# Kernel optimization log

Hardware: AMD Instinct MI355X
Metric: run time of the kernel (lower is better)

Reference implementation:

```python
import jax, jax.numpy as jnp
import numpy as np

N = 16384            # mesh vertices at full resolution (level 3)
DEG = 8              # avg nonzeros per Laplacian row
F_IN = 3
F_HID = 128
LOCAL_LAYERS = 15
LEVEL_N = [N >> (3 - l) for l in range(4)]  # [2048, 4096, 8192, 16384]


def setup_inputs():
    key = jax.random.key(0)
    ks = iter(jax.random.split(key, 48))
    d = {}
    d['inputs'] = jax.random.normal(next(ks), (1, N, F_IN), dtype=jnp.float32)
    d['mask0'] = jnp.ones((1, N, 1), jnp.float32)
    d['mask1'] = jnp.ones((1, N, 1), jnp.float32)
    for l, n in enumerate(LEVEL_N):
        e = DEG * n
        d[f'lap{l}_rows'] = jnp.sort(jax.random.randint(next(ks), (e,), 0, n, dtype=jnp.int32))
        d[f'lap{l}_cols'] = jax.random.randint(next(ks), (e,), 0, n, dtype=jnp.int32)
        d[f'lap{l}_vals'] = 0.25 * jax.random.normal(next(ks), (e,), dtype=jnp.float32)
    e = DEG * N
    d['L_rows'] = jnp.sort(jax.random.randint(next(ks), (e,), 0, N, dtype=jnp.int32))
    d['L_cols'] = jax.random.randint(next(ks), (e,), 0, N, dtype=jnp.int32)
    d['L_vals'] = 0.25 * jax.random.normal(next(ks), (e,), dtype=jnp.float32)
    s_in = 0.577   # ~1/sqrt(F_IN)
    s_h = 0.0625   # 1/sqrt(2*F_HID)
    d['g_conv1_W'] = s_in * jax.random.normal(next(ks), (F_IN, F_HID), dtype=jnp.float32)
    d['g_conv1_b'] = jnp.zeros((F_HID,), jnp.float32)
    d['g_down_W'] = s_h * jax.random.normal(next(ks), (3, 2, 2 * F_HID, F_HID), dtype=jnp.float32)
    d['g_down_b'] = jnp.zeros((3, 2, F_HID), jnp.float32)
    d['g_lap0_W'] = s_h * jax.random.normal(next(ks), (2, 2 * F_HID, F_HID), dtype=jnp.float32)
    d['g_lap0_b'] = jnp.zeros((2, F_HID), jnp.float32)
    d['g_up_W'] = s_h * jax.random.normal(next(ks), (3, 2, 2 * F_HID, F_HID), dtype=jnp.float32)
    d['g_up_b'] = jnp.zeros((3, 2, F_HID), jnp.float32)
    d['g_conv2_W'] = s_h * jax.random.normal(next(ks), (F_HID, 2), dtype=jnp.float32)
    d['g_conv2_b'] = jnp.zeros((2,), jnp.float32)
    d['l_conv1_W'] = s_in * jax.random.normal(next(ks), (F_IN, F_HID), dtype=jnp.float32)
    d['l_conv1_b'] = jnp.zeros((F_HID,), jnp.float32)
    d['l_rn_W'] = s_h * jax.random.normal(next(ks), (LOCAL_LAYERS, 2, 2 * F_HID, F_HID), dtype=jnp.float32)
    d['l_rn_b'] = jnp.zeros((LOCAL_LAYERS, 2, F_HID), jnp.float32)
    d['l_conv2_W'] = s_h * jax.random.normal(next(ks), (F_HID, 1), dtype=jnp.float32)
    d['l_conv2_b'] = jnp.zeros((1,), jnp.float32)
    return d


def _spmm(rows, cols, vals, x):
    # y = L @ x for an n x n COO Laplacian; x: [1, n, f] (batch=1, sparse mm path)
    y = jax.ops.segment_sum(vals[:, None] * x[0, cols, :], rows, num_segments=x.shape[1])
    return y[None]


def _lap_block(lap, x, Ws, bs):
    # _LapResNet2 (num_outputs == num_inputs == 128): elu -> cat([x, Lx]) -> 1x1 conv, residual
    inp = x
    for j in range(Ws.shape[0]):
        x = jax.nn.elu(x)
        x = jnp.concatenate([x, _spmm(lap[0], lap[1], lap[2], x)], axis=-1) @ Ws[j] + bs[j]
    return x + inp


def _avg_block(mask, x, Ws, bs):
    # _AvgResNet2: elu -> cat([x, masked global average]) -> 1x1 conv, residual
    inp = x
    denom = jnp.sum(mask, axis=1, keepdims=True)
    for j in range(Ws.shape[0]):
        x = jax.nn.elu(x)
        avg = jnp.sum(x * mask, axis=1, keepdims=True) / denom
        x = jnp.concatenate([x, jnp.broadcast_to(avg, x.shape)], axis=-1) @ Ws[j] + bs[j]
    return x + inp


def _maxpool2(x):
    # MaxPool1d(2, stride=2) along the node dim
    b, n, f = x.shape
    return x.reshape(b, n // 2, 2, f).max(axis=2)


def _forward(inputs, mask0, mask1, lap0_vals, lap1_vals, lap2_vals, lap3_vals, L_vals,
             g_conv1_W, g_conv1_b, g_down_W, g_down_b, g_lap0_W, g_lap0_b,
             g_up_W, g_up_b, g_conv2_W, g_conv2_b,
             l_conv1_W, l_conv1_b, l_rn_W, l_rn_b, l_conv2_W, l_conv2_b,
             lap0_rows, lap0_cols, lap1_rows, lap1_cols, lap2_rows, lap2_cols,
             lap3_rows, lap3_cols, L_rows, L_cols):
    laps = [(lap0_rows, lap0_cols, lap0_vals), (lap1_rows, lap1_cols, lap1_vals),
            (lap2_rows, lap2_cols, lap2_vals), (lap3_rows, lap3_cols, lap3_vals)]
    # ----- global net: EfficientCascade (naive max-pool cascade, 4 levels) -----
    # (mask0 is only max-pooled in torch; _LapResNet2 ignores it, so it does not affect math)
    x = inputs @ g_conv1_W + g_conv1_b
    down = []
    for k, i in enumerate((3, 2, 1)):
        down.append(x)
        x = _lap_block(laps[i], x, g_down_W[k], g_down_b[k])
        x = _maxpool2(x)
    x = _lap_block(laps[0], x, g_lap0_W, g_lap0_b)
    for i in (1, 2, 3):
        x = jnp.repeat(x, 2, axis=1)      # F.interpolate(scale_factor=2), nearest
        x = x + down[-i]                  # channels equal -> plain residual add
        x = _lap_block(laps[i], x, g_up_W[i - 1], g_up_b[i - 1])
    swg = jax.nn.elu(x) @ g_conv2_W + g_conv2_b + inputs[:, :, :2]  # + repeating_expand(inputs, 2)
    # ----- local net: LapDeepModel, 15 alternating Lap / global-avg resblocks -----
    L = (L_rows, L_cols, L_vals)
    y = inputs @ l_conv1_W + l_conv1_b
    for i in range(LOCAL_LAYERS):
        if i % 2 == 0:
            y = _lap_block(L, y, l_rn_W[i], l_rn_b[i])
        else:
            y = _avg_block(mask1, y, l_rn_W[i], l_rn_b[i])
    score_local = jax.nn.elu(y) @ l_conv2_W + l_conv2_b + inputs[:, :, :1]
    # ----- combine -----
    score_global = swg[:, :, :1]
    weight_global = jax.nn.sigmoid(swg[:, :, :-1])  # out_features=1 -> same first channel
    score_final = weight_global * score_global + (1.0 - weight_global) * score_local
    return jnp.concatenate([score_global, score_local, score_final], axis=1)


def reference(inputs, mask0, mask1, lap0_rows, lap0_cols, lap0_vals,
              lap1_rows, lap1_cols, lap1_vals, lap2_rows, lap2_cols, lap2_vals,
              lap3_rows, lap3_cols, lap3_vals, L_rows, L_cols, L_vals,
              g_conv1_W, g_conv1_b, g_down_W, g_down_b, g_lap0_W, g_lap0_b,
              g_up_W, g_up_b, g_conv2_W, g_conv2_b,
              l_conv1_W, l_conv1_b, l_rn_W, l_rn_b, l_conv2_W, l_conv2_b):
    return _forward(inputs, mask0, mask1, lap0_vals, lap1_vals, lap2_vals, lap3_vals, L_vals,
                    g_conv1_W, g_conv1_b, g_down_W, g_down_b, g_lap0_W, g_lap0_b,
                    g_up_W, g_up_b, g_conv2_W, g_conv2_b,
                    l_conv1_W, l_conv1_b, l_rn_W, l_rn_b, l_conv2_W, l_conv2_b,
                    lap0_rows, lap0_cols, lap1_rows, lap1_cols, lap2_rows, lap2_cols,
                    lap3_rows, lap3_cols, L_rows, L_cols)
```

## Files before the change

kernel.cpp:

```cpp
#include <hip/hip_runtime.h>

#define F 128
#define SPAD 136
#define NR 32

typedef __attribute__((ext_vector_type(8))) short short8;
typedef __attribute__((ext_vector_type(16))) float f32x16;
typedef unsigned long long ull;

__device__ __forceinline__ float elu_f(float x) {
    return x > 0.f ? x : __expf(x) - 1.f;
}
__device__ __forceinline__ ushort f2bf(float x) {
    unsigned u = __float_as_uint(x);
    u = (u + 0x7FFFu + ((u >> 16) & 1u)) >> 16;
    return (ushort)u;
}
__device__ __forceinline__ float bf2f(ushort u) {
    return __uint_as_float((unsigned)u << 16);
}
__device__ __forceinline__ void bfma8(float* a, float v, short8 u) {
#pragma unroll
    for (int i = 0; i < 8; ++i) a[i] += v * bf2f((ushort)u[i]);
}

struct SetupArgs {
    const float* ws0; const float* ws1; const float* ws2; const float* ws3;
    ushort* wd0; ushort* wd1; ushort* wd2; ushort* wd3;
    const int* rows0; const int* rows1; const int* rows2; const int* rows3; const int* rows4;
    int* rp0; int* rp1; int* rp2; int* rp3; int* rp4;
    const float* mask; float* den; float* acc;
    const float* in; const float* Wg; const float* bg; const float* Wl; const float* bl;
    float* og; ushort* eg; float* ol; ushort* el;
};

__global__ __launch_bounds__(256) void setup_conv1(SetupArgs s) {
    __shared__ ushort tile[16384];
    int b = blockIdx.x, t = threadIdx.x;
    if (b >= 274) {
        int id = (b - 274) * 256 + t;
        int r = id >> 7, c = id & 127;
        float x0 = s.in[r * 3 + 0], x1 = s.in[r * 3 + 1], x2 = s.in[r * 3 + 2];
        float g = x0 * s.Wg[c] + x1 * s.Wg[F + c] + x2 * s.Wg[2 * F + c] + s.bg[c];
        float lo = x0 * s.Wl[c] + x1 * s.Wl[F + c] + x2 * s.Wl[2 * F + c] + s.bl[c];
        s.og[id] = g;  s.eg[id] = f2bf(elu_f(g));
        s.ol[id] = lo; s.el[id] = f2bf(elu_f(lo));
    } else if (b < 88) {
        const float* src; ushort* dst; int lb;
        if (b < 12)      { src = s.ws0; dst = s.wd0; lb = b; }
        else if (b < 16) { src = s.ws1; dst = s.wd1; lb = b - 12; }
        else if (b < 28) { src = s.ws2; dst = s.wd2; lb = b - 16; }
        else             { src = s.ws3; dst = s.wd3; lb = b - 28; }
        src += (size_t)lb * 16384; dst += (size_t)lb * 16384;
        for (int idx = t; idx < 16384; idx += 256) {
            int k = idx >> 7, nn = idx & 127;
            int k0 = k >> 4, rk = k & 15, j = rk & 7, lh = rk >> 3;
            int n0 = nn >> 5, ll = nn & 31;
            tile[((k0 * 4 + n0) * 64 + lh * 32 + ll) * 8 + j] = f2bf(src[idx]);
        }
        __syncthreads();
        ull* td = (ull*)dst; const ull* ts = (const ull*)tile;
        for (int i = t; i < 4096; i += 256) td[i] = ts[i];
    } else if (b < 273) {
        int tid = (b - 88) * 256 + t;
        const int ns[5] = {2048, 4096, 8192, 16384, 16384};
        const int es[5] = {16384, 32768, 65536, 131072, 131072};
        const int* rowsA[5] = {s.rows0, s.rows1, s.rows2, s.rows3, s.rows4};
        int* rpA[5] = {s.rp0, s.rp1, s.rp2, s.rp3, s.rp4};
        int base = 0;
        for (int lv = 0; lv < 5; ++lv) {
            int cnt = ns[lv] + 1;
            if (tid < base + cnt) {
                int r = tid - base;
                const int* rows = rowsA[lv]; int e = es[lv];
                int lo = 0, hi = e;
                while (lo < hi) { int mid = (lo + hi) >> 1; if (rows[mid] < r) lo = mid + 1; else hi = mid; }
                rpA[lv][r] = lo;
                return;
            }
            base += cnt;
        }
    } else {
        __shared__ float red[256];
        float ssum = 0.f;
        for (int i = t; i < 16384; i += 256) ssum += s.mask[i];
        red[t] = ssum; __syncthreads();
        for (int st = 128; st > 0; st >>= 1) { if (t < st) red[t] += red[t + st]; __syncthreads(); }
        if (t == 0) s.den[0] = red[0];
        for (int i = t; i < 14336; i += 256) s.acc[i] = 0.f;
    }
}

struct LArgs {
    const ushort* EA; const float* RES; float* OUT; ushort* EAOUT;
    const int* rowptr; const int* cols; const float* vals;
    const ushort* Wp; const float* bias;
    const float* accin; const float* den;
    const float* mask; float* accout;
    float* EO; ushort* EE; const float* SKIP;
    int epi;
    int fin;
    const float* Finp; const ushort* FEB0;
    const float* FgW2; const float* Fgb2; const float* FlW2; const float* Flb2;
    float* Fout;
};

__device__ __forceinline__ void layer_body(const LArgs& a, int blk, ushort* SS, float* FS) {
    const int t = threadIdx.x;
    const int rbase = blk * NR;
    const int w = t >> 6, l = t & 63, m = l & 31, kh = l >> 5;
    const int col = w * 32 + m;
    const bool lap = (a.rowptr != nullptr);
    const bool avg = (a.accin != nullptr);

    short8 afrag[8];
    {
        const ushort* ear = a.EA + (size_t)(rbase + m) * F + kh * 8;
#pragma unroll
        for (int ki = 0; ki < 8; ++ki) afrag[ki] = *(const short8*)(ear + ki * 16);
    }

    if (lap) {
        const int grp = t >> 3, l8 = t & 7;
        const short8* EA8 = (const short8*)a.EA;
        const int chunk = l8 * 2;
        int row = rbase + grp;
        int e0 = a.rowptr[row], e1 = a.rowptr[row + 1];
        float acc0[16], acc1[16];
#pragma unroll
        for (int i = 0; i < 16; ++i) { acc0[i] = 0.f; acc1[i] = 0.f; }
        int e = e0;
        for (; e + 4 <= e1; e += 4) {
            int c0 = a.cols[e + 0], c1 = a.cols[e + 1], c2 = a.cols[e + 2], c3 = a.cols[e + 3];
            float v0 = a.vals[e + 0], v1 = a.vals[e + 1], v2 = a.vals[e + 2], v3 = a.vals[e + 3];
            short8 u0a = EA8[(size_t)c0 * 16 + chunk], u0b = EA8[(size_t)c0 * 16 + chunk + 1];
            short8 u1a = EA8[(size_t)c1 * 16 + chunk], u1b = EA8[(size_t)c1 * 16 + chunk + 1];
            short8 u2a = EA8[(size_t)c2 * 16 + chunk], u2b = EA8[(size_t)c2 * 16 + chunk + 1];
            short8 u3a = EA8[(size_t)c3 * 16 + chunk], u3b = EA8[(size_t)c3 * 16 + chunk + 1];
            bfma8(acc0, v0, u0a); bfma8(acc0 + 8, v0, u0b);
            bfma8(acc1, v1, u1a); bfma8(acc1 + 8, v1, u1b);
            bfma8(acc0, v2, u2a); bfma8(acc0 + 8, v2, u2b);
            bfma8(acc1, v3, u3a); bfma8(acc1 + 8, v3, u3b);
        }
        for (; e < e1; ++e) {
            int cc = a.cols[e];
            float v = a.vals[e];
            short8 ua = EA8[(size_t)cc * 16 + chunk], ub = EA8[(size_t)cc * 16 + chunk + 1];
            bfma8(acc0, v, ua); bfma8(acc0 + 8, v, ub);
        }
        short8 s0, s1;
#pragma unroll
        for (int i = 0; i < 8; ++i) {
            s0[i] = (short)f2bf(acc0[i] + acc1[i]);
            s1[i] = (short)f2bf(acc0[8 + i] + acc1[8 + i]);
        }
        *(short8*)(&SS[grp * SPAD + l8 * 16]) = s0;
        *(short8*)(&SS[grp * SPAD + l8 * 16 + 8]) = s1;
        __syncthreads();
    } else if (avg) {
        if (t < 128) {
            float s = 0.f;
#pragma unroll
            for (int r = 0; r < 8; ++r) s += a.accin[r * 128 + t];
            SS[t] = f2bf(s / a.den[0]);
        }
        __syncthreads();
    }

    f32x16 acc;
#pragma unroll
    for (int i = 0; i < 16; ++i) acc[i] = 0.f;
#pragma unroll
    for (int ki = 0; ki < 8; ++ki) {
        short8 b = *(const short8*)(a.Wp + (size_t)(((ki * 4 + w) * 64 + l) * 8));
        acc = __builtin_amdgcn_mfma_f32_32x32x16_bf16(afrag[ki], b, acc, 0, 0, 0);
    }
    if (lap || avg) {
        const ushort* esr = lap ? &SS[m * SPAD + kh * 8] : &SS[kh * 8];
#pragma unroll
        for (int ki = 0; ki < 8; ++ki) {
            short8 aa = *(const short8*)(esr + ki * 16);
            short8 b = *(const short8*)(a.Wp + 16384 + (size_t)(((ki * 4 + w) * 64 + l) * 8));
            acc = __builtin_amdgcn_mfma_f32_32x32x16_bf16(aa, b, acc, 0, 0, 0);
        }
    }

    const float bv = a.bias[col];
    float outv[16];
#pragma unroll
    for (int reg = 0; reg < 16; ++reg) {
        int r = (reg & 3) + 8 * (reg >> 2) + 4 * kh;
        size_t rg = (size_t)(rbase + r);
        float v = acc[reg] + bv;
        if (a.RES) v += a.RES[rg * F + col];
        outv[reg] = v;
        if (a.OUT) a.OUT[rg * F + col] = v;
        if (a.EAOUT) a.EAOUT[rg * F + col] = f2bf(elu_f(v));
    }
    if (a.accout) {
        float p = 0.f;
#pragma unroll
        for (int reg = 0; reg < 16; ++reg) {
            int r = (reg & 3) + 8 * (reg >> 2) + 4 * kh;
            p += elu_f(outv[reg]) * a.mask[rbase + r];
        }
        p += __shfl_xor(p, 32, 64);
        if (l < 32) atomicAdd(a.accout + (blk & 7) * 128 + col, p);
    }
    if (a.epi == 1) {
        int rb2 = rbase >> 1;
#pragma unroll
        for (int q = 0; q < 4; ++q)
#pragma unroll
            for (int e2 = 0; e2 < 2; ++e2) {
                float pv = fmaxf(outv[q * 4 + e2 * 2], outv[q * 4 + e2 * 2 + 1]);
                size_t idx = (size_t)(rb2 + q * 4 + kh * 2 + e2) * F + col;
                a.EO[idx] = pv;
                a.EE[idx] = f2bf(elu_f(pv));
            }
    } else if (a.epi == 2) {
#pragma unroll
        for (int reg = 0; reg < 16; ++reg) {
            int r = (reg & 3) + 8 * (reg >> 2) + 4 * kh;
            size_t R0 = (size_t)(2 * (rbase + r)) * F + col;
            float v0 = outv[reg] + a.SKIP[R0];
            float v1 = outv[reg] + a.SKIP[R0 + F];
            a.EO[R0] = v0;     a.EO[R0 + F] = v1;
            a.EE[R0] = f2bf(elu_f(v0)); a.EE[R0 + F] = f2bf(elu_f(v1));
        }
    }
    if (a.fin) {
        __syncthreads();
        if (t < 64) FS[t] = 0.f;
        __syncthreads();
        const float lw = a.FlW2[col];
#pragma unroll
        for (int reg = 0; reg < 16; ++reg) {
            int r = (reg & 3) + 8 * (reg >> 2) + 4 * kh;
            atomicAdd(&FS[r], elu_f(outv[reg]) * lw);
        }
        for (int idx = t; idx < 32 * 128; idx += 256) {
            int r = idx >> 7, cc = idx & 127;
            atomicAdd(&FS[32 + r], bf2f(a.FEB0[(size_t)(rbase + r) * F + cc]) * a.FgW2[2 * cc]);
        }
        __syncthreads();
        if (t < 32) {
            int rg = rbase + t;
            float base = a.Finp[rg * 3 + 0];
            float sg = FS[32 + t] + a.Fgb2[0] + base;
            float sl = FS[t] + a.Flb2[0] + base;
            float wg = 1.f / (1.f + __expf(-sg));
            a.Fout[rg] = sg;
            a.Fout[16384 + rg] = sl;
            a.Fout[32768 + rg] = wg * sg + (1.f - wg) * sl;
        }
    }
}

__global__ __launch_bounds__(256)
void dual_layer(LArgs A, LArgs B, int nA) {
    __shared__ ushort SS[NR * SPAD];
    __shared__ float FS[64];
    bool isA = (int)blockIdx.x < nA;
    const LArgs& a = isA ? A : B;
    int blk = isA ? blockIdx.x : blockIdx.x - nA;
    layer_body(a, blk, SS, FS);
}

extern "C" void kernel_launch(void* const* d_in, const int* in_sizes, int n_in,
                              void* d_out, int out_size, void* d_ws, size_t ws_size,
                              hipStream_t stream) {
    (void)in_sizes; (void)n_in; (void)out_size; (void)ws_size;
    const float* inputs = (const float*)d_in[0];
    const float* mask1  = (const float*)d_in[2];
    const int*   lrows[5] = {(const int*)d_in[3], (const int*)d_in[6], (const int*)d_in[9],
                             (const int*)d_in[12], (const int*)d_in[15]};
    const int*   lcols[5] = {(const int*)d_in[4], (const int*)d_in[7], (const int*)d_in[10],
                             (const int*)d_in[13], (const int*)d_in[16]};
    const float* lvals[5] = {(const float*)d_in[5], (const float*)d_in[8], (const float*)d_in[11],
                             (const float*)d_in[14], (const float*)d_in[17]};
    const float* gW1 = (const float*)d_in[18];
    const float* gb1 = (const float*)d_in[19];
    const float* gdW = (const float*)d_in[20];
    const float* gdb = (const float*)d_in[21];
    const float* glW = (const float*)d_in[22];
    const float* glb = (const float*)d_in[23];
    const float* guW = (const float*)d_in[24];
    const float* gub = (const float*)d_in[25];
    const float* gW2 = (const float*)d_in[26];
    const float* gb2 = (const float*)d_in[27];
    const float* lW1 = (const float*)d_in[28];
    const float* lb1 = (const float*)d_in[29];
    const float* lrW = (const float*)d_in[30];
    const float* lrb = (const float*)d_in[31];
    const float* lW2 = (const float*)d_in[32];
    const float* lb2 = (const float*)d_in[33];
    float* out = (float*)d_out;

    const int N = 16384;
    const int nlev[5] = {2048, 4096, 8192, 16384, 16384};

    char* ws = (char*)d_ws;
    size_t off = 0;
    auto alloc = [&](size_t bytes) -> char* {
        char* p = ws + off;
        off = (off + bytes + 255) & ~(size_t)255;
        return p;
    };
    float* BUF0 = (float*)alloc((size_t)N * F * 4);
    float* GU   = (float*)alloc((size_t)N * F * 4);
    float* G2   = (float*)alloc((size_t)N * F * 4);
    float* D8   = (float*)alloc((size_t)8192 * F * 4);
    float* D4   = (float*)alloc((size_t)4096 * F * 4);
    float* D2   = (float*)alloc((size_t)2048 * F * 4);
    float* LB   = (float*)alloc((size_t)N * F * 4);
    ushort* EB0 = (ushort*)alloc((size_t)N * F * 2);
    ushort* EG1 = (ushort*)alloc((size_t)N * F * 2);
    ushort* EG2 = (ushort*)alloc((size_t)N * F * 2);
    ushort* ED8 = (ushort*)alloc((size_t)8192 * F * 2);
    ushort* ED4 = (ushort*)alloc((size_t)4096 * F * 2);
    ushort* ED2 = (ushort*)alloc((size_t)2048 * F * 2);
    ushort* LE1 = (ushort*)alloc((size_t)N * F * 2);
    ushort* LE2 = (ushort*)alloc((size_t)N * F * 2);
    int* rp[5];
    for (int i = 0; i < 5; ++i) rp[i] = (int*)alloc((size_t)(nlev[i] + 1) * 4);
    float* ACC = (float*)alloc((size_t)14 * 8 * 128 * 4);
    float* DEN = (float*)alloc(4);
    ushort* Pd = (ushort*)alloc((size_t)12 * 16384 * 2);
    ushort* Pl = (ushort*)alloc((size_t)4  * 16384 * 2);
    ushort* Pu = (ushort*)alloc((size_t)12 * 16384 * 2);
    ushort* Pr = (ushort*)alloc((size_t)60 * 16384 * 2);

    SetupArgs sa;
    sa.ws0 = gdW; sa.ws1 = glW; sa.ws2 = guW; sa.ws3 = lrW;
    sa.wd0 = Pd;  sa.wd1 = Pl;  sa.wd2 = Pu;  sa.wd3 = Pr;
    sa.rows0 = lrows[0]; sa.rows1 = lrows[1]; sa.rows2 = lrows[2];
    sa.rows3 = lrows[3]; sa.rows4 = lrows[4];
    sa.rp0 = rp[0]; sa.rp1 = rp[1]; sa.rp2 = rp[2]; sa.rp3 = rp[3]; sa.rp4 = rp[4];
    sa.mask = mask1; sa.den = DEN; sa.acc = ACC;
    sa.in = inputs; sa.Wg = gW1; sa.bg = gb1; sa.Wl = lW1; sa.bl = lb1;
    sa.og = BUF0; sa.eg = EB0; sa.ol = LB; sa.el = LE1;
    setup_conv1<<<274 + 8192, 256, 0, stream>>>(sa);

    const size_t PSZ = 2 * 16384;

    auto mkL = [&](const ushort* ea, const float* res, float* o, ushort* eao,
                   int lv, const ushort* wp, const float* bias, float* accout,
                   int epi, float* eo, ushort* ee, const float* skip,
                   const float* accin, int fin) {
        LArgs x;
        x.EA = ea; x.RES = res; x.OUT = o; x.EAOUT = eao;
        x.rowptr = (lv >= 0) ? rp[lv] : nullptr;
        x.cols = (lv >= 0) ? lcols[lv] : nullptr;
        x.vals = (lv >= 0) ? lvals[lv] : nullptr;
        x.Wp = wp; x.bias = bias;
        x.accin = accin; x.den = DEN;
        x.mask = mask1; x.accout = accout;
        x.EO = eo; x.EE = ee; x.SKIP = skip; x.epi = epi;
        x.fin = fin;
        x.Finp = inputs; x.FEB0 = EB0;
        x.FgW2 = gW2; x.Fgb2 = gb2; x.FlW2 = lW2; x.Flb2 = lb2; x.Fout = out;
        return x;
    };

    LArgs gs[14]; int gn[14];
    gs[0]  = mkL(EB0, 0, 0, EG1, 3, Pd + 0 * PSZ, gdb + 0,   0, 0, 0, 0, 0, 0, 0);  gn[0]  = 16384;
    gs[1]  = mkL(EG1, BUF0, 0, 0, 3, Pd + 1 * PSZ, gdb + 128, 0, 1, D8, ED8, 0, 0, 0); gn[1] = 16384;
    gs[2]  = mkL(ED8, 0, 0, EG1, 2, Pd + 2 * PSZ, gdb + 256, 0, 0, 0, 0, 0, 0, 0);  gn[2]  = 8192;
    gs[3]  = mkL(EG1, D8, 0, 0, 2, Pd + 3 * PSZ, gdb + 384, 0, 1, D4, ED4, 0, 0, 0); gn[3]  = 8192;
    gs[4]  = mkL(ED4, 0, 0, EG1, 1, Pd + 4 * PSZ, gdb + 512, 0, 0, 0, 0, 0, 0, 0);  gn[4]  = 4096;
    gs[5]  = mkL(EG1, D4, 0, 0, 1, Pd + 5 * PSZ, gdb + 640, 0, 1, D2, ED2, 0, 0, 0); gn[5]  = 4096;
    gs[6]  = mkL(ED2, 0, 0, EG1, 0, Pl + 0 * PSZ, glb + 0,   0, 0, 0, 0, 0, 0, 0);  gn[6]  = 2048;
    gs[7]  = mkL(EG1, D2, 0, 0, 0, Pl + 1 * PSZ, glb + 128, 0, 2, GU, EG2, D4, 0, 0); gn[7] = 2048;
    gs[8]  = mkL(EG2, 0, 0, EG1, 1, Pu + 0 * PSZ, gub + 0,   0, 0, 0, 0, 0, 0, 0);  gn[8]  = 4096;
    gs[9]  = mkL(EG1, GU, 0, 0, 1, Pu + 1 * PSZ, gub + 128, 0, 2, G2, EG2, D8, 0, 0); gn[9] = 4096;
    gs[10] = mkL(EG2, 0, 0, EG1, 2, Pu + 2 * PSZ, gub + 256, 0, 0, 0, 0, 0, 0, 0);  gn[10] = 8192;
    gs[11] = mkL(EG1, G2, 0, 0, 2, Pu + 3 * PSZ, gub + 384, 0, 2, GU, EG2, BUF0, 0, 0); gn[11] = 8192;
    gs[12] = mkL(EG2, 0, 0, EG1, 3, Pu + 4 * PSZ, gub + 512, 0, 0, 0, 0, 0, 0, 0);  gn[12] = 16384;
    gs[13] = mkL(EG1, GU, 0, EB0, 3, Pu + 5 * PSZ, gub + 640, 0, 0, 0, 0, 0, 0, 0); gn[13] = 16384;

    int gi = 0;
    auto launchLap = [&](const LArgs& loc) {
        if (gi < 14) {
            int na = gn[gi] / NR;
            dual_layer<<<na + 512, 256, 0, stream>>>(gs[gi], loc, na);
            ++gi;
        } else {
            dual_layer<<<512, 256, 0, stream>>>(loc, loc, 512);
        }
    };

    for (int i = 0; i < 15; ++i) {
        const ushort* P1 = Pr + (size_t)(2 * i) * PSZ;
        const ushort* P2 = Pr + (size_t)(2 * i + 1) * PSZ;
        const float* b1 = lrb + (size_t)i * 256;
        const float* b2 = b1 + 128;
        if ((i & 1) == 0) {
            LArgs s1 = mkL(LE1, 0, 0, LE2, 4, P1, b1, 0, 0, 0, 0, 0, 0, 0);
            float* accout = (i <= 12) ? (ACC + (size_t)i * 1024) : nullptr;
            int fin = (i == 14);
            LArgs s2 = mkL(LE2, LB, fin ? nullptr : LB, fin ? nullptr : LE1, 4,
                           P2, b2, accout, 0, 0, 0, 0, 0, fin);
            launchLap(s1);
            launchLap(s2);
        } else {
            LArgs s1 = mkL(LE1, 0, 0, LE2, -1, P1, b1, ACC + (size_t)i * 1024,
                           0, 0, 0, 0, ACC + (size_t)(i - 1) * 1024, 0);
            LArgs s2 = mkL(LE2, LB, LB, LE1, -1, P2, b2, 0,
                           0, 0, 0, 0, ACC + (size_t)i * 1024, 0);
            launchLap(s1);
            launchLap(s2);
        }
    }
}
```

Baseline: 680.1 us.

## Stage Laplacian neighbor rows into LDS via global_load_lds before SpMM

Replaces the per-thread direct gather of bf16 neighbor rows in the sparse Laplacian product with a block-cooperative staging scheme. Each wave issues global_load_lds for chunks of 112 edges into a shared buffer, then threads accumulate from LDS. The aim is to turn scattered vector loads into asynchronous direct-to-LDS transfers. In exchange it adds about 30KB of LDS per block, extra barriers per chunk, and serial shuffle-driven issue, which may cut occupancy. A buffer named GU is renamed to avoid clashing with a new typedef.

```diff
diff --git a/kernel.cpp b/kernel.cpp
--- a/kernel.cpp
+++ b/kernel.cpp
@@ -3,10 +3,15 @@
 #define F 128
 #define SPAD 136
 #define NR 32
+#define CH 112
+#define EPW 28
+#define GPAD 136
 
 typedef __attribute__((ext_vector_type(8))) short short8;
 typedef __attribute__((ext_vector_type(16))) float f32x16;
 typedef unsigned long long ull;
+typedef __attribute__((address_space(1))) const unsigned GU;
+typedef __attribute__((address_space(3))) unsigned LU;
 
 __device__ __forceinline__ float elu_f(float x) {
     return x > 0.f ? x : __expf(x) - 1.f;
@@ -105,7 +110,8 @@
     float* Fout;
 };
 
-__device__ __forceinline__ void layer_body(const LArgs& a, int blk, ushort* SS, float* FS) {
+__device__ __forceinline__ void layer_body(const LArgs& a, int blk, ushort* SS,
+                                           float* FS, ushort* STG) {
     const int t = threadIdx.x;
     const int rbase = blk * NR;
     const int w = t >> 6, l = t & 63, m = l & 31, kh = l >> 5;
@@ -122,37 +128,48 @@
 
     if (lap) {
         const int grp = t >> 3, l8 = t & 7;
-        const short8* EA8 = (const short8*)a.EA;
-        const int chunk = l8 * 2;
+        const int lane = t & 63;
         int row = rbase + grp;
-        int e0 = a.rowptr[row], e1 = a.rowptr[row + 1];
-        float acc0[16], acc1[16];
-#pragma unroll
-        for (int i = 0; i < 16; ++i) { acc0[i] = 0.f; acc1[i] = 0.f; }
-        int e = e0;
-        for (; e + 4 <= e1; e += 4) {
-            int c0 = a.cols[e + 0], c1 = a.cols[e + 1], c2 = a.cols[e + 2], c3 = a.cols[e + 3];
-            float v0 = a.vals[e + 0], v1 = a.vals[e + 1], v2 = a.vals[e + 2], v3 = a.vals[e + 3];
-            short8 u0a = EA8[(size_t)c0 * 16 + chunk], u0b = EA8[(size_t)c0 * 16 + chunk + 1];
-            short8 u1a = EA8[(size_t)c1 * 16 + chunk], u1b = EA8[(size_t)c1 * 16 + chunk + 1];
-            short8 u2a = EA8[(size_t)c2 * 16 + chunk], u2b = EA8[(size_t)c2 * 16 + chunk + 1];
-            short8 u3a = EA8[(size_t)c3 * 16 + chunk], u3b = EA8[(size_t)c3 * 16 + chunk + 1];
-            bfma8(acc0, v0, u0a); bfma8(acc0 + 8, v0, u0b);
-            bfma8(acc1, v1, u1a); bfma8(acc1 + 8, v1, u1b);
-            bfma8(acc0, v2, u2a); bfma8(acc0 + 8, v2, u2b);
-            bfma8(acc1, v3, u3a); bfma8(acc1 + 8, v3, u3b);
-        }
-        for (; e < e1; ++e) {
-            int cc = a.cols[e];
-            float v = a.vals[e];
-            short8 ua = EA8[(size_t)cc * 16 + chunk], ub = EA8[(size_t)cc * 16 + chunk + 1];
-            bfma8(acc0, v, ua); bfma8(acc0 + 8, v, ub);
+        int re0 = a.rowptr[row], re1 = a.rowptr[row + 1];
+        int b0 = a.rowptr[rbase];
+        int b1 = a.rowptr[rbase + NR];
+        float acc0[16];
+#pragma unroll
+        for (int i = 0; i < 16; ++i) acc0[i] = 0.f;
+
+        for (int cs = b0; cs < b1; cs += CH) {
+            int ce = cs + CH; if (ce > b1) ce = b1;
+            int cnt = ce - cs;
+            int wbeg = w * EPW;
+            int wcnt = cnt - wbeg;
+            if (wcnt > EPW) wcnt = EPW;
+            if (wcnt < 0) wcnt = 0;
+            int colv = 0;
+            if (lane < wcnt) colv = a.cols[cs + wbeg + lane];
+            for (int j = 0; j < wcnt; ++j) {
+                int c = __shfl(colv, j, 64);
+                __builtin_amdgcn_global_load_lds(
+                    (GU*)(a.EA + (size_t)c * F) + lane,
+                    (LU*)&STG[(wbeg + j) * GPAD], 4, 0, 0);
+            }
+            __builtin_amdgcn_s_waitcnt(0);
+            __syncthreads();
+            int ae = re0 > cs ? re0 : cs;
+            int be = re1 < ce ? re1 : ce;
+            for (int e = ae; e < be; ++e) {
+                float v = a.vals[e];
+                const ushort* lr = &STG[(e - cs) * GPAD + l8 * 16];
+                short8 ua = *(const short8*)(lr);
+                short8 ub = *(const short8*)(lr + 8);
+                bfma8(acc0, v, ua); bfma8(acc0 + 8, v, ub);
+            }
+            __syncthreads();
         }
         short8 s0, s1;
 #pragma unroll
         for (int i = 0; i < 8; ++i) {
-            s0[i] = (short)f2bf(acc0[i] + acc1[i]);
-            s1[i] = (short)f2bf(acc0[8 + i] + acc1[8 + i]);
+            s0[i] = (short)f2bf(acc0[i]);
+            s1[i] = (short)f2bf(acc0[8 + i]);
         }
         *(short8*)(&SS[grp * SPAD + l8 * 16]) = s0;
         *(short8*)(&SS[grp * SPAD + l8 * 16 + 8]) = s1;
@@ -259,12 +276,13 @@
 
 __global__ __launch_bounds__(256)
 void dual_layer(LArgs A, LArgs B, int nA) {
+    __shared__ ushort STG[CH * GPAD];
     __shared__ ushort SS[NR * SPAD];
     __shared__ float FS[64];
     bool isA = (int)blockIdx.x < nA;
     const LArgs& a = isA ? A : B;
     int blk = isA ? blockIdx.x : blockIdx.x - nA;
-    layer_body(a, blk, SS, FS);
+    layer_body(a, blk, SS, FS, STG);
 }
 
 extern "C" void kernel_launch(void* const* d_in, const int* in_sizes, int n_in,
@@ -308,7 +326,7 @@
         return p;
     };
     float* BUF0 = (float*)alloc((size_t)N * F * 4);
-    float* GU   = (float*)alloc((size_t)N * F * 4);
+    float* GU2  = (float*)alloc((size_t)N * F * 4);
     float* G2   = (float*)alloc((size_t)N * F * 4);
     float* D8   = (float*)alloc((size_t)8192 * F * 4);
     float* D4   = (float*)alloc((size_t)4096 * F * 4);
@@ -371,13 +389,13 @@
     gs[4]  = mkL(ED4, 0, 0, EG1, 1, Pd + 4 * PSZ, gdb + 512, 0, 0, 0, 0, 0, 0, 0);  gn[4]  = 4096;
     gs[5]  = mkL(EG1, D4, 0, 0, 1, Pd + 5 * PSZ, gdb + 640, 0, 1, D2, ED2, 0, 0, 0); gn[5]  = 4096;
     gs[6]  = mkL(ED2, 0, 0, EG1, 0, Pl + 0 * PSZ, glb + 0,   0, 0, 0, 0, 0, 0, 0);  gn[6]  = 2048;
-    gs[7]  = mkL(EG1, D2, 0, 0, 0, Pl + 1 * PSZ, glb + 128, 0, 2, GU, EG2, D4, 0, 0); gn[7] = 2048;
+    gs[7]  = mkL(EG1, D2, 0, 0, 0, Pl + 1 * PSZ, glb + 128, 0, 2, GU2, EG2, D4, 0, 0); gn[7] = 2048;
     gs[8]  = mkL(EG2, 0, 0, EG1, 1, Pu + 0 * PSZ, gub + 0,   0, 0, 0, 0, 0, 0, 0);  gn[8]  = 4096;
-    gs[9]  = mkL(EG1, GU, 0, 0, 1, Pu + 1 * PSZ, gub + 128, 0, 2, G2, EG2, D8, 0, 0); gn[9] = 4096;
+    gs[9]  = mkL(EG1, GU2, 0, 0, 1, Pu + 1 * PSZ, gub + 128, 0, 2, G2, EG2, D8, 0, 0); gn[9] = 4096;
     gs[10] = mkL(EG2, 0, 0, EG1, 2, Pu + 2 * PSZ, gub + 256, 0, 0, 0, 0, 0, 0, 0);  gn[10] = 8192;
-    gs[11] = mkL(EG1, G2, 0, 0, 2, Pu + 3 * PSZ, gub + 384, 0, 2, GU, EG2, BUF0, 0, 0); gn[11] = 8192;
+    gs[11] = mkL(EG1, G2, 0, 0, 2, Pu + 3 * PSZ, gub + 384, 0, 2, GU2, EG2, BUF0, 0, 0); gn[11] = 8192;
     gs[12] = mkL(EG2, 0, 0, EG1, 3, Pu + 4 * PSZ, gub + 512, 0, 0, 0, 0, 0, 0, 0);  gn[12] = 16384;
-    gs[13] = mkL(EG1, GU, 0, EB0, 3, Pu + 5 * PSZ, gub + 640, 0, 0, 0, 0, 0, 0, 0); gn[13] = 16384;
+    gs[13] = mkL(EG1, GU2, 0, EB0, 3, Pu + 5 * PSZ, gub + 640, 0, 0, 0, 0, 0, 0, 0); gn[13] = 16384;
 
     int gi = 0;
     auto launchLap = [&](const LArgs& loc) {
```

Result: slower. 810.2 us (+19.1%).
